# Kernel tuning notes

Hardware: AMD Instinct MI355X
Metric: run time of the kernel (lower is better)

The kernel has to match this reference:

```python
import jax, jax.numpy as jnp
import numpy as np

N, D = 512, 128


def setup_inputs() -> dict:
    key = jax.random.key(0)
    k1, k2 = jax.random.split(key)
    source = jax.random.normal(k1, (N, D), dtype=jnp.float32)
    target = jax.random.normal(k2, (N, D), dtype=jnp.float32)
    return {"source": source, "target": target}


def _distance_matrix(x):
    # pairwise squared-euclidean distances, same broadcast form as torch source
    return jnp.sum((x[:, None, :] - x[None, :, :]) ** 2, axis=-1)  # [n,n]


def reference(source, target):
    n = source.shape[0]
    C_s = _distance_matrix(source)  # [n,n]
    C_t = _distance_matrix(target)  # [n,n]
    # cost[i,j,k] = |C_s[i,j] - C_t[i,k]|  -> [n,n,n]
    cost = jnp.abs(C_s[:, :, None] - C_t[:, None, :])
    # transport_plan = outer(1/n, 1/n) is constant uniform 1/n^2;
    # the torch loop recomputes the identical value max_iter times, so one pass suffices.
    plan = jnp.float32(1.0) / (n * n)
    gw_dist = jnp.sum(cost * cost) * plan
    return gw_dist
```

## Files before the change

### kernel.cpp

```cpp
#include <hip/hip_runtime.h>

#define N 512
#define D 128


__device__ __forceinline__ double wave_reduce_add(double v) {
    #pragma unroll
    for (int off = 32; off > 0; off >>= 1)
        v += __shfl_down(v, off, 64);
    return v;
}

__global__ __launch_bounds__(512) void gw_dist(
    const float* __restrict__ src, const float* __restrict__ tgt,
    double* __restrict__ rs, double* __restrict__ ss)
{
    __shared__ float  tile[32 * 513];
    __shared__ double red[8][8];

    const int b   = blockIdx.x;
    const int m   = b >> 7;
    const int iq  = b & 127;
    const int i0  = iq * 4;
    const int tid = threadIdx.x;

    const float*  X  = m ? tgt : src;
    const float4* X4 = reinterpret_cast<const float4*>(X);
    const float* r0  = X + (i0 + 0) * D;
    const float* r1  = X + (i0 + 1) * D;
    const float* r2  = X + (i0 + 2) * D;
    const float* r3  = X + (i0 + 3) * D;

    const int jhome = tid >> 3;
    const int d4    = tid & 7;

    float a0 = 0.f, a1 = 0.f, a2 = 0.f, a3 = 0.f;

    for (int c = 0; c < 4; ++c) {
        #pragma unroll
        for (int p = 0; p < 8; ++p) {
            int jr = p * 64 + jhome;
            float4 v = X4[jr * (D / 4) + c * 8 + d4];
            tile[(d4 * 4 + 0) * 513 + jr] = v.x;
            tile[(d4 * 4 + 1) * 513 + jr] = v.y;
            tile[(d4 * 4 + 2) * 513 + jr] = v.z;
            tile[(d4 * 4 + 3) * 513 + jr] = v.w;
        }
        __syncthreads();

        #pragma unroll
        for (int dd = 0; dd < 32; ++dd) {
            float v = tile[dd * 513 + tid];
            int   d = c * 32 + dd;
            float e;
            e = r0[d] - v; a0 += e * e;
            e = r1[d] - v; a1 += e * e;
            e = r2[d] - v; a2 += e * e;
            e = r3[d] - v; a3 += e * e;
        }
        __syncthreads();
    }

    double q[8];
    q[0] = (double)a0; q[1] = (double)a1; q[2] = (double)a2; q[3] = (double)a3;
    q[4] = (double)a0 * (double)a0;
    q[5] = (double)a1 * (double)a1;
    q[6] = (double)a2 * (double)a2;
    q[7] = (double)a3 * (double)a3;

    const int wave = tid >> 6;
    const int lane = tid & 63;
    #pragma unroll
    for (int k = 0; k < 8; ++k) {
        double v = wave_reduce_add(q[k]);
        if (lane == 0) red[wave][k] = v;
    }
    __syncthreads();

    if (tid == 0) {
        #pragma unroll
        for (int k = 0; k < 4; ++k) {
            double rsk = 0.0, ssk = 0.0;
            #pragma unroll
            for (int w = 0; w < 8; ++w) { rsk += red[w][k]; ssk += red[w][k + 4]; }
            rs[m * N + i0 + k] = rsk;
            ss[m * N + i0 + k] = ssk;
        }
    }
}

__global__ __launch_bounds__(512) void gw_finalize(
    const double* __restrict__ rs, const double* __restrict__ ss,
    float* __restrict__ out)
{
    const int i = threadIdx.x;

    const double rs_s = rs[0 * N + i];
    const double rs_t = rs[1 * N + i];
    const double ss_s = ss[0 * N + i];
    const double ss_t = ss[1 * N + i];

    double v = (double)N * (ss_s + ss_t) - 2.0 * rs_s * rs_t;
    v = wave_reduce_add(v);

    __shared__ double sm[8];
    const int wave = i >> 6;
    const int lane = i & 63;
    if (lane == 0) sm[wave] = v;
    __syncthreads();

    if (i == 0) {
        double total = 0.0;
        #pragma unroll
        for (int w = 0; w < 8; ++w) total += sm[w];
        out[0] = (float)(total / ((double)N * (double)N));
    }
}

extern "C" void kernel_launch(void* const* d_in, const int* in_sizes, int n_in,
                              void* d_out, int out_size, void* d_ws, size_t ws_size,
                              hipStream_t stream) {
    const float* src = (const float*)d_in[0];
    const float* tgt = (const float*)d_in[1];
    float* out = (float*)d_out;

    double* rs = (double*)d_ws;
    double* ss = rs + 2 * N;

    gw_dist    <<<dim3(256), dim3(512), 0, stream>>>(src, tgt, rs, ss);
    gw_finalize<<<dim3(1),   dim3(512), 0, stream>>>(rs, ss, out);
}
```

Measured before the change: 18.90 us.

## Retile distance kernel: 8 rows per block, half j-range, split-D threads, swizzled LDS

Each block now loads a 256-row half of the matrix into LDS once, using an XOR swizzle instead of padding, and computes 8 query rows rather than 4. The two thread halves each cover half of the feature dimension and are combined through shared memory. The per-block partial sums are written per j-half, and the finalize kernel adds the two halves. This removes the chunked load/sync loop and raises arithmetic reuse per loaded element. The cost is a 128KB LDS tile limiting occupancy to one block per CU, plus an extra reduction step where half the threads go idle.

```diff
diff --git a/kernel.cpp b/kernel.cpp
--- a/kernel.cpp
+++ b/kernel.cpp
@@ -15,76 +15,106 @@
     const float* __restrict__ src, const float* __restrict__ tgt,
     double* __restrict__ rs, double* __restrict__ ss)
 {
-    __shared__ float  tile[32 * 513];
-    __shared__ double red[8][8];
+    __shared__ float  tile[D * 256];
+    __shared__ float  part[256][9];
+    __shared__ double red[8][16];
 
-    const int b   = blockIdx.x;
-    const int m   = b >> 7;
-    const int iq  = b & 127;
-    const int i0  = iq * 4;
-    const int tid = threadIdx.x;
+    const int b    = blockIdx.x;
+    const int m    = b >> 7;
+    const int ioct = (b & 127) >> 1;
+    const int jh   = b & 1;
+    const int t    = threadIdx.x;
+    const int jl   = t & 255;
+    const int dh   = t >> 8;
+    const int i0   = ioct * 8;
+    const int j0   = jh * 256;
 
     const float*  X  = m ? tgt : src;
-    const float4* X4 = reinterpret_cast<const float4*>(X);
-    const float* r0  = X + (i0 + 0) * D;
-    const float* r1  = X + (i0 + 1) * D;
-    const float* r2  = X + (i0 + 2) * D;
-    const float* r3  = X + (i0 + 3) * D;
+    const float4* X4 = reinterpret_cast<const float4*>(X + j0 * D);
 
-    const int jhome = tid >> 3;
-    const int d4    = tid & 7;
+    #pragma unroll
+    for (int p = 0; p < 16; ++p) {
+        int f  = t + p * 512;
+        int jr = f >> 5;
+        int s  = f & 31;
+        float4 v = X4[f];
+        int col = jr ^ s;
+        col = (jr & ~31) | ((jr ^ s) & 31);
+        tile[(4 * s + 0) * 256 + col] = v.x;
+        tile[(4 * s + 1) * 256 + col] = v.y;
+        tile[(4 * s + 2) * 256 + col] = v.z;
+        tile[(4 * s + 3) * 256 + col] = v.w;
+    }
+    __syncthreads();
 
+    const int dbase = dh * 64;
     float a0 = 0.f, a1 = 0.f, a2 = 0.f, a3 = 0.f;
+    float a4 = 0.f, a5 = 0.f, a6 = 0.f, a7 = 0.f;
+    const float* r0 = X + (i0 + 0) * D + dbase;
+    const float* r1 = X + (i0 + 1) * D + dbase;
+    const float* r2 = X + (i0 + 2) * D + dbase;
+    const float* r3 = X + (i0 + 3) * D + dbase;
+    const float* r4 = X + (i0 + 4) * D + dbase;
+    const float* r5 = X + (i0 + 5) * D + dbase;
+    const float* r6 = X + (i0 + 6) * D + dbase;
+    const float* r7 = X + (i0 + 7) * D + dbase;
 
-    for (int c = 0; c < 4; ++c) {
-        #pragma unroll
-        for (int p = 0; p < 8; ++p) {
-            int jr = p * 64 + jhome;
-            float4 v = X4[jr * (D / 4) + c * 8 + d4];
-            tile[(d4 * 4 + 0) * 513 + jr] = v.x;
-            tile[(d4 * 4 + 1) * 513 + jr] = v.y;
-            tile[(d4 * 4 + 2) * 513 + jr] = v.z;
-            tile[(d4 * 4 + 3) * 513 + jr] = v.w;
-        }
-        __syncthreads();
-
-        #pragma unroll
-        for (int dd = 0; dd < 32; ++dd) {
-            float v = tile[dd * 513 + tid];
-            int   d = c * 32 + dd;
-            float e;
-            e = r0[d] - v; a0 += e * e;
-            e = r1[d] - v; a1 += e * e;
-            e = r2[d] - v; a2 += e * e;
-            e = r3[d] - v; a3 += e * e;
-        }
-        __syncthreads();
+    #pragma unroll 4
+    for (int dd = 0; dd < 64; ++dd) {
+        int d = dbase + dd;
+        int col = (jl & ~31) | ((jl ^ (d >> 2)) & 31);
+        float v = tile[d * 256 + col];
+        float e;
+        e = r0[dd] - v; a0 += e * e;
+        e = r1[dd] - v; a1 += e * e;
+        e = r2[dd] - v; a2 += e * e;
+        e = r3[dd] - v; a3 += e * e;
+        e = r4[dd] - v; a4 += e * e;
+        e = r5[dd] - v; a5 += e * e;
+        e = r6[dd] - v; a6 += e * e;
+        e = r7[dd] - v; a7 += e * e;
     }
 
-    double q[8];
-    q[0] = (double)a0; q[1] = (double)a1; q[2] = (double)a2; q[3] = (double)a3;
-    q[4] = (double)a0 * (double)a0;
-    q[5] = (double)a1 * (double)a1;
-    q[6] = (double)a2 * (double)a2;
-    q[7] = (double)a3 * (double)a3;
+    if (dh == 1) {
+        part[jl][0] = a0; part[jl][1] = a1; part[jl][2] = a2; part[jl][3] = a3;
+        part[jl][4] = a4; part[jl][5] = a5; part[jl][6] = a6; part[jl][7] = a7;
+    }
+    __syncthreads();
 
-    const int wave = tid >> 6;
-    const int lane = tid & 63;
+    double q[16];
+    if (dh == 0) {
+        float c;
+        c = a0 + part[jl][0]; q[0] = (double)c; q[8]  = (double)c * (double)c;
+        c = a1 + part[jl][1]; q[1] = (double)c; q[9]  = (double)c * (double)c;
+        c = a2 + part[jl][2]; q[2] = (double)c; q[10] = (double)c * (double)c;
+        c = a3 + part[jl][3]; q[3] = (double)c; q[11] = (double)c * (double)c;
+        c = a4 + part[jl][4]; q[4] = (double)c; q[12] = (double)c * (double)c;
+        c = a5 + part[jl][5]; q[5] = (double)c; q[13] = (double)c * (double)c;
+        c = a6 + part[jl][6]; q[6] = (double)c; q[14] = (double)c * (double)c;
+        c = a7 + part[jl][7]; q[7] = (double)c; q[15] = (double)c * (double)c;
+    } else {
+        #pragma unroll
+        for (int k = 0; k < 16; ++k) q[k] = 0.0;
+    }
+
+    const int wave = t >> 6;
+    const int lane = t & 63;
     #pragma unroll
-    for (int k = 0; k < 8; ++k) {
+    for (int k = 0; k < 16; ++k) {
         double v = wave_reduce_add(q[k]);
         if (lane == 0) red[wave][k] = v;
     }
     __syncthreads();
 
-    if (tid == 0) {
+    if (t == 0) {
+        const int base = ((jh << 1) | m) * N + i0;
         #pragma unroll
-        for (int k = 0; k < 4; ++k) {
+        for (int k = 0; k < 8; ++k) {
             double rsk = 0.0, ssk = 0.0;
             #pragma unroll
-            for (int w = 0; w < 8; ++w) { rsk += red[w][k]; ssk += red[w][k + 4]; }
-            rs[m * N + i0 + k] = rsk;
-            ss[m * N + i0 + k] = ssk;
+            for (int w = 0; w < 8; ++w) { rsk += red[w][k]; ssk += red[w][k + 8]; }
+            rs[base + k] = rsk;
+            ss[base + k] = ssk;
         }
     }
 }
@@ -95,10 +125,10 @@
 {
     const int i = threadIdx.x;
 
-    const double rs_s = rs[0 * N + i];
-    const double rs_t = rs[1 * N + i];
-    const double ss_s = ss[0 * N + i];
-    const double ss_t = ss[1 * N + i];
+    const double rs_s = rs[0 * N + i] + rs[2 * N + i];
+    const double rs_t = rs[1 * N + i] + rs[3 * N + i];
+    const double ss_s = ss[0 * N + i] + ss[2 * N + i];
+    const double ss_t = ss[1 * N + i] + ss[3 * N + i];
 
     double v = (double)N * (ss_s + ss_t) - 2.0 * rs_s * rs_t;
     v = wave_reduce_add(v);
@@ -125,7 +155,7 @@
     float* out = (float*)d_out;
 
     double* rs = (double*)d_ws;
-    double* ss = rs + 2 * N;
+    double* ss = rs + 4 * N;
 
     gw_dist    <<<dim3(256), dim3(512), 0, stream>>>(src, tgt, rs, ss);
     gw_finalize<<<dim3(1),   dim3(512), 0, stream>>>(rs, ss, out);
```

After: 22.46 us, median of 2. +18.8%, slower.
